# Kernel optimization log

Measured on AMD Instinct MI355X. Metric: run time of the kernel, lower is better.

The kernel has to match this reference:

```python
import jax, jax.numpy as jnp
import numpy as np

D = 1024
H = 16
HD = D // H
B = 8
S = 1024


def setup_inputs() -> dict:
    key = jax.random.key(0)
    ks = jax.random.split(key, 12)
    std = 0.02
    inp = {
        "x": jax.random.normal(ks[0], (B, S, D), jnp.float32),
        "rel_pos_enc": jax.random.normal(ks[1], (S, HD), jnp.float32) * std,
        "attention_mask": jax.random.randint(ks[2], (B, S), 0, 2, jnp.int32),
        "Wq": jax.random.normal(ks[3], (D, D), jnp.float32) * std,
        "bq": jnp.zeros((D,), jnp.float32),
        "Wk": jax.random.normal(ks[4], (D, D), jnp.float32) * std,
        "bk": jnp.zeros((D,), jnp.float32),
        "Wv": jax.random.normal(ks[5], (D, D), jnp.float32) * std,
        "bv": jnp.zeros((D,), jnp.float32),
        "Wo": jax.random.normal(ks[6], (D, D), jnp.float32) * std,
        "bo": jnp.zeros((D,), jnp.float32),
    }
    return inp


def reference(x, rel_pos_enc, attention_mask, Wq, bq, Wk, bk, Wv, bv, Wo, bo):
    b, s, d = x.shape
    scale = HD ** -0.5
    # projections + split heads -> [B, H, S, hd]
    q = (x @ Wq + bq).reshape(b, s, H, HD).transpose(0, 2, 1, 3)
    k = (x @ Wk + bk).reshape(b, s, H, HD).transpose(0, 2, 1, 3)
    v = (x @ Wv + bv).reshape(b, s, H, HD).transpose(0, 2, 1, 3)
    # content scores [B,H,S,S]
    scores = jnp.einsum("bhsd,bhtd->bhst", q, k) * scale
    # additive relative-position bias: q . rel_pos_enc[t]  -> [B,H,S,S]
    scores = scores + jnp.einsum("bhsd,td->bhst", q, rel_pos_enc)
    # key-padding mask [B,S] -> [B,1,1,S]
    scores = jnp.where(attention_mask[:, None, None, :] == 0, -jnp.inf, scores)
    attn = jax.nn.softmax(scores, axis=-1)
    ctx = jnp.einsum("bhst,bhtd->bhsd", attn, v)
    ctx = ctx.transpose(0, 2, 1, 3).reshape(b, s, d)
    return ctx @ Wo + bo
```

## Files before the change

kernel.cpp:

```cpp
#include <hip/hip_runtime.h>

#define DD 1024
#define HH 16
#define HDD 64
#define BBATCH 8
#define SS 1024
#define NROW (BBATCH*SS)
#define PSTR 72

typedef _Float16 f16x8 __attribute__((ext_vector_type(8)));
typedef _Float16 f16x4 __attribute__((ext_vector_type(4)));
typedef float    f32x4 __attribute__((ext_vector_type(4)));

__device__ __forceinline__ void async_cp16(const void* g, void* l) {
    __builtin_amdgcn_global_load_lds(
        (const __attribute__((address_space(1))) void*)g,
        (__attribute__((address_space(3))) void*)l, 16, 0, 0);
}

__global__ __launch_bounds__(256) void conv_x_kernel(
    const float* __restrict__ x, _Float16* __restrict__ xh)
{
    size_t i8 = ((size_t)blockIdx.x * 256 + threadIdx.x) * 8;
    float4 v0 = *(const float4*)&x[i8];
    float4 v1 = *(const float4*)&x[i8 + 4];
    float vf[8] = {v0.x, v0.y, v0.z, v0.w, v1.x, v1.y, v1.z, v1.w};
    f16x8 hv;
    #pragma unroll
    for (int c = 0; c < 8; c++) hv[c] = (_Float16)vf[c];
    *(f16x8*)&xh[i8] = hv;
}

__global__ __launch_bounds__(256) void conv_w_kernel(
    const float* __restrict__ Wq, const float* __restrict__ Wk,
    const float* __restrict__ Wv, const float* __restrict__ Wo,
    _Float16* __restrict__ wt, _Float16* __restrict__ wot)
{
    __shared__ float T[64][65];
    const int z = blockIdx.z;
    const float* src = (z == 0) ? Wq : (z == 1) ? Wk : (z == 2) ? Wv : Wo;
    _Float16* dh = (z < 3) ? wt + (size_t)z * 1024 * 1024 : wot;
    const int k0 = blockIdx.x * 64, n0 = blockIdx.y * 64;
    const int tid = threadIdx.x;

    #pragma unroll
    for (int rep = 0; rep < 4; rep++) {
        int e = rep * 256 + tid;
        int kr = e >> 4, nc = (e & 15) * 4;
        *(float4*)&T[kr][nc] = *(const float4*)&src[(size_t)(k0 + kr) * 1024 + n0 + nc];
    }
    __syncthreads();
    #pragma unroll
    for (int rep = 0; rep < 4; rep++) {
        int e = rep * 256 + tid;
        int nr = e >> 4, kc = (e & 15) * 4;
        f16x4 hv;
        #pragma unroll
        for (int c = 0; c < 4; c++) hv[c] = (_Float16)T[kc + c][nr];
        *(f16x4*)&dh[(size_t)(n0 + nr) * 1024 + k0 + kc] = hv;
    }
}

__global__ __launch_bounds__(256) void gemm_f16(
    const _Float16* __restrict__ Ag, const _Float16* __restrict__ Bg,
    const float* __restrict__ b0, const float* __restrict__ b1,
    const float* __restrict__ b2, const float* __restrict__ rel,
    _Float16* __restrict__ oq, _Float16* __restrict__ okh,
    _Float16* __restrict__ ovt, float* __restrict__ dOut, int mode)
{
    __shared__ _Float16 smem[8192];
    _Float16* Ah = smem;
    _Float16* Bh = smem + 4096;

    const int tid = threadIdx.x;
    const int w = tid >> 6, l = tid & 63;
    const int lane15 = l & 15, quad = l >> 4;
    const int rm = (w >> 1) * 64, cn = (w & 1) * 64;
    const size_t r0 = (size_t)blockIdx.y * 128;
    const size_t n0 = (size_t)blockIdx.x * 128;

    const int lrow = l >> 2;
    const int lko  = (l & 3) * 8;
    const int ch0 = 2 * w, ch1 = 2 * w + 1;

    f32x4 acc[4][4] = {};

    for (int ks = 0; ks < 32; ks++) {
        const size_t kofs = (size_t)ks * 32 + lko;
        __syncthreads();
        {
            const size_t ga0 = (r0 + ch0 * 16 + lrow) * 1024 + kofs;
            const size_t ga1 = (r0 + ch1 * 16 + lrow) * 1024 + kofs;
            const size_t gb0 = (n0 + ch0 * 16 + lrow) * 1024 + kofs;
            const size_t gb1 = (n0 + ch1 * 16 + lrow) * 1024 + kofs;
            async_cp16(&Ag[ga0], &Ah[ch0 * 512]);
            async_cp16(&Ag[ga1], &Ah[ch1 * 512]);
            async_cp16(&Bg[gb0], &Bh[ch0 * 512]);
            async_cp16(&Bg[gb1], &Bh[ch1 * 512]);
        }
        __syncthreads();

        f16x8 ah[4], bh4[4];
        #pragma unroll
        for (int ii = 0; ii < 4; ii++)
            ah[ii] = *(const f16x8*)&Ah[(rm + ii * 16 + lane15) * 32 + quad * 8];
        #pragma unroll
        for (int jj = 0; jj < 4; jj++)
            bh4[jj] = *(const f16x8*)&Bh[(cn + jj * 16 + lane15) * 32 + quad * 8];
        #pragma unroll
        for (int ii = 0; ii < 4; ii++)
            #pragma unroll
            for (int jj = 0; jj < 4; jj++)
                acc[ii][jj] = __builtin_amdgcn_mfma_f32_16x16x32_f16(
                    ah[ii], bh4[jj], acc[ii][jj], 0, 0, 0);
    }

    if (mode == 0) {
        const int z = blockIdx.x >> 3;
        const float* bias = (z == 0) ? b0 : (z == 1) ? b1 : b2;
        const int nbase = (blockIdx.x & 7) * 128 + cn;
        #pragma unroll
        for (int ii = 0; ii < 4; ii++)
            #pragma unroll
            for (int jj = 0; jj < 4; jj++) {
                int nc = nbase + jj * 16 + lane15;
                int hh = nc >> 6, hd = nc & 63;
                float bsv = bias[nc];
                #pragma unroll
                for (int r = 0; r < 4; r++) {
                    int gr = (int)r0 + rm + ii * 16 + quad * 4 + r;
                    int bb = gr >> 10, s = gr & 1023;
                    float val = acc[ii][jj][r] + bsv;
                    size_t hidx = (((size_t)bb * HH + hh) * SS + s) * HDD + hd;
                    if (z == 0) {
                        oq[hidx] = (_Float16)val;
                    } else if (z == 1) {
                        okh[hidx] = (_Float16)(val * 0.125f + rel[s * HDD + hd]);
                    } else {
                        ovt[(((size_t)bb * HH + hh) * HDD + hd) * SS + s] = (_Float16)val;
                    }
                }
            }
    } else {
        #pragma unroll
        for (int ii = 0; ii < 4; ii++)
            #pragma unroll
            for (int jj = 0; jj < 4; jj++) {
                int nc = (int)n0 + cn + jj * 16 + lane15;
                float bsv = b0[nc];
                #pragma unroll
                for (int r = 0; r < 4; r++) {
                    int gr = (int)r0 + rm + ii * 16 + quad * 4 + r;
                    dOut[(size_t)gr * DD + nc] = acc[ii][jj][r] + bsv;
                }
            }
    }
}

__global__ __launch_bounds__(512, 4) void attn_mfma(
    const _Float16* __restrict__ qh, const _Float16* __restrict__ kh,
    const _Float16* __restrict__ vt, const int* __restrict__ mask,
    _Float16* __restrict__ ctx)
{
    __shared__ _Float16 Kbuf[2][64 * PSTR];
    __shared__ _Float16 Vbuf[2][64 * PSTR];
    __shared__ _Float16 Ps[128 * PSTR];
    __shared__ float maddL[1024];

    const int tid = threadIdx.x;
    const int w = tid >> 6, l = tid & 63;
    const int lane15 = l & 15, quad = l >> 4;
    const int id = blockIdx.x;
    const int qt = id >> 7;
    const int bh = id & 127;
    const int b = bh >> 4, h = bh & 15;
    const size_t kbase0 = (size_t)bh * SS;
    const size_t vbase0 = (size_t)bh * HDD;
    const int qrow_blk = qt * 128 + w * 16;

    for (int i = tid; i < 1024; i += 512)
        maddL[i] = (mask[b * SS + i] == 0) ? -1e30f : 0.0f;

    f16x8 qf[2];
    #pragma unroll
    for (int ks = 0; ks < 2; ks++)
        qf[ks] = *(const f16x8*)&qh[(kbase0 + qrow_blk + lane15) * HDD + ks * 32 + quad * 8];

    f16x8 vone;
    #pragma unroll
    for (int j = 0; j < 8; j++) vone[j] = (lane15 == 0) ? (_Float16)1.0f : (_Float16)0.0f;

    f32x4 O[5] = {};

    const int grow = tid >> 3;
    const int gcc  = (tid & 7) * 8;
    const _Float16* kp = &kh[(kbase0 + grow) * HDD + gcc];
    const _Float16* vp = &vt[(vbase0 + grow) * SS + gcc];
    f16x8 kreg = *(const f16x8*)kp;
    f16x8 vreg = *(const f16x8*)vp;

    int p = 0;
    for (int kt = 0; kt < 16; kt++) {
        *(f16x8*)&Kbuf[p][grow * PSTR + gcc] = kreg;
        *(f16x8*)&Vbuf[p][grow * PSTR + gcc] = vreg;
        __syncthreads();

        const int nkt = (kt + 1) & 15;
        kreg = *(const f16x8*)(kp + (size_t)nkt * 64 * HDD);
        vreg = *(const f16x8*)(vp + (size_t)nkt * 64);

        const int t0 = kt * 64;

        f32x4 S[4];
        #pragma unroll
        for (int nt = 0; nt < 4; nt++) {
            f16x8 kf0 = *(const f16x8*)&Kbuf[p][(nt * 16 + lane15) * PSTR + quad * 8];
            f16x8 kf1 = *(const f16x8*)&Kbuf[p][(nt * 16 + lane15) * PSTR + 32 + quad * 8];
            f32x4 c = {};
            c = __builtin_amdgcn_mfma_f32_16x16x32_f16(qf[0], kf0, c, 0, 0, 0);
            c = __builtin_amdgcn_mfma_f32_16x16x32_f16(qf[1], kf1, c, 0, 0, 0);
            S[nt] = c;
        }

        const int rowb = w * 16 + quad * 4;
        #pragma unroll
        for (int nt = 0; nt < 4; nt++) {
            float madd = maddL[t0 + nt * 16 + lane15] - 3.0f;
            int colp = (nt * 16 + lane15 + 16 * quad) & 63;
            #pragma unroll
            for (int r = 0; r < 4; r++)
                Ps[(rowb + r) * PSTR + colp] = (_Float16)__expf(S[nt][r] + madd);
        }

        const int swz = 16 * (lane15 >> 2);
        #pragma unroll
        for (int ks2 = 0; ks2 < 2; ks2++) {
            int colp = (ks2 * 32 + quad * 8 + swz) & 63;
            f16x8 pf = *(const f16x8*)&Ps[(w * 16 + lane15) * PSTR + colp];
            #pragma unroll
            for (int nd = 0; nd < 4; nd++) {
                f16x8 vf = *(const f16x8*)&Vbuf[p][(nd * 16 + lane15) * PSTR + ks2 * 32 + quad * 8];
                O[nd] = __builtin_amdgcn_mfma_f32_16x16x32_f16(pf, vf, O[nd], 0, 0, 0);
            }
            O[4] = __builtin_amdgcn_mfma_f32_16x16x32_f16(pf, vone, O[4], 0, 0, 0);
        }
        p ^= 1;
    }

    float linv[4];
    #pragma unroll
    for (int r = 0; r < 4; r++) {
        float lsum = __shfl(O[4][r], l & 48, 64);
        linv[r] = 1.0f / lsum;
    }
    #pragma unroll
    for (int nd = 0; nd < 4; nd++) {
        int d = nd * 16 + lane15;
        #pragma unroll
        for (int r = 0; r < 4; r++) {
            int qrow = qt * 128 + w * 16 + quad * 4 + r;
            ctx[((size_t)b * SS + qrow) * DD + h * HDD + d] =
                (_Float16)(O[nd][r] * linv[r]);
        }
    }
}

extern "C" void kernel_launch(void* const* d_in, const int* in_sizes, int n_in,
                              void* d_out, int out_size, void* d_ws, size_t ws_size,
                              hipStream_t stream) {
    const float* x    = (const float*)d_in[0];
    const float* rel  = (const float*)d_in[1];
    const int*   mask = (const int*)d_in[2];
    const float* Wq = (const float*)d_in[3];  const float* bq = (const float*)d_in[4];
    const float* Wk = (const float*)d_in[5];  const float* bk = (const float*)d_in[6];
    const float* Wv = (const float*)d_in[7];  const float* bv = (const float*)d_in[8];
    const float* Wo = (const float*)d_in[9];  const float* bo = (const float*)d_in[10];
    float* out = (float*)d_out;

    const size_t XN = (size_t)NROW * DD;
    char* p = (char*)d_ws;
    _Float16* xh  = (_Float16*)p; p += XN * 2;
    _Float16* wt  = (_Float16*)p; p += (size_t)3072 * 1024 * 2;
    _Float16* wot = (_Float16*)p; p += (size_t)1024 * 1024 * 2;
    _Float16* qhp = (_Float16*)p; p += XN * 2;
    _Float16* khp = (_Float16*)p; p += XN * 2;
    _Float16* vtp = (_Float16*)p; p += XN * 2;
    _Float16* ctx = xh;

    conv_x_kernel<<<dim3((unsigned)(XN / 2048)), 256, 0, stream>>>(x, xh);
    conv_w_kernel<<<dim3(16, 16, 4), 256, 0, stream>>>(Wq, Wk, Wv, Wo, wt, wot);
    gemm_f16<<<dim3(24, 64), 256, 0, stream>>>(
        xh, wt, bq, bk, bv, rel, qhp, khp, vtp, nullptr, 0);
    attn_mfma<<<dim3(1024), 512, 0, stream>>>(
        qhp, khp, vtp, mask, ctx);
    gemm_f16<<<dim3(8, 64), 256, 0, stream>>>(
        ctx, wot, bo, nullptr, nullptr, nullptr,
        nullptr, nullptr, nullptr, out, 1);
}
```

Measured before the change: 316.2 us.

## Double GEMM K-tile to 64 and XOR-swizzle LDS layout

The f16 GEMM now loads a 128x64 K-slice of A and B per iteration instead of 128x32. This halves the number of barrier pairs and loop iterations. The LDS layout stores each 16-byte chunk at a position XORed with the row index, so the fragment reads for MFMA avoid bank conflicts. LDS use doubles to 32 KB per block, which may reduce occupancy.

Result: faster. 306.3 us (-3.1%).

```diff
diff --git a/kernel.cpp b/kernel.cpp
--- a/kernel.cpp
+++ b/kernel.cpp
@@ -68,9 +68,9 @@
     _Float16* __restrict__ oq, _Float16* __restrict__ okh,
     _Float16* __restrict__ ovt, float* __restrict__ dOut, int mode)
 {
-    __shared__ _Float16 smem[8192];
+    __shared__ _Float16 smem[16384];
     _Float16* Ah = smem;
-    _Float16* Bh = smem + 4096;
+    _Float16* Bh = smem + 8192;
 
     const int tid = threadIdx.x;
     const int w = tid >> 6, l = tid & 63;
@@ -79,40 +79,48 @@
     const size_t r0 = (size_t)blockIdx.y * 128;
     const size_t n0 = (size_t)blockIdx.x * 128;
 
-    const int lrow = l >> 2;
-    const int lko  = (l & 3) * 8;
-    const int ch0 = 2 * w, ch1 = 2 * w + 1;
+    const int srow = tid >> 3;
+    const int schp = tid & 7;
+    const int sch  = schp ^ (srow & 7);
 
     f32x4 acc[4][4] = {};
 
-    for (int ks = 0; ks < 32; ks++) {
-        const size_t kofs = (size_t)ks * 32 + lko;
+    for (int ks = 0; ks < 16; ks++) {
+        const int kbase = ks * 64;
         __syncthreads();
-        {
-            const size_t ga0 = (r0 + ch0 * 16 + lrow) * 1024 + kofs;
-            const size_t ga1 = (r0 + ch1 * 16 + lrow) * 1024 + kofs;
-            const size_t gb0 = (n0 + ch0 * 16 + lrow) * 1024 + kofs;
-            const size_t gb1 = (n0 + ch1 * 16 + lrow) * 1024 + kofs;
-            async_cp16(&Ag[ga0], &Ah[ch0 * 512]);
-            async_cp16(&Ag[ga1], &Ah[ch1 * 512]);
-            async_cp16(&Bg[gb0], &Bh[ch0 * 512]);
-            async_cp16(&Bg[gb1], &Bh[ch1 * 512]);
+        #pragma unroll
+        for (int i = 0; i < 4; i++) {
+            int row = i * 32 + srow;
+            int s = row * 8 + schp;
+            const size_t ga = (r0 + row) * 1024 + kbase + sch * 8;
+            const size_t gb = (n0 + row) * 1024 + kbase + sch * 8;
+            async_cp16(&Ag[ga], &Ah[s * 8]);
+            async_cp16(&Bg[gb], &Bh[s * 8]);
         }
         __syncthreads();
 
-        f16x8 ah[4], bh4[4];
-        #pragma unroll
-        for (int ii = 0; ii < 4; ii++)
-            ah[ii] = *(const f16x8*)&Ah[(rm + ii * 16 + lane15) * 32 + quad * 8];
-        #pragma unroll
-        for (int jj = 0; jj < 4; jj++)
-            bh4[jj] = *(const f16x8*)&Bh[(cn + jj * 16 + lane15) * 32 + quad * 8];
-        #pragma unroll
-        for (int ii = 0; ii < 4; ii++)
-            #pragma unroll
-            for (int jj = 0; jj < 4; jj++)
-                acc[ii][jj] = __builtin_amdgcn_mfma_f32_16x16x32_f16(
-                    ah[ii], bh4[jj], acc[ii][jj], 0, 0, 0);
+        #pragma unroll
+        for (int ksub = 0; ksub < 2; ksub++) {
+            f16x8 ah[4], bh4[4];
+            #pragma unroll
+            for (int ii = 0; ii < 4; ii++) {
+                int row = rm + ii * 16 + lane15;
+                int chp = (ksub * 4 + quad) ^ (row & 7);
+                ah[ii] = *(const f16x8*)&Ah[row * 64 + chp * 8];
+            }
+            #pragma unroll
+            for (int jj = 0; jj < 4; jj++) {
+                int col = cn + jj * 16 + lane15;
+                int chp = (ksub * 4 + quad) ^ (col & 7);
+                bh4[jj] = *(const f16x8*)&Bh[col * 64 + chp * 8];
+            }
+            #pragma unroll
+            for (int ii = 0; ii < 4; ii++)
+                #pragma unroll
+                for (int jj = 0; jj < 4; jj++)
+                    acc[ii][jj] = __builtin_amdgcn_mfma_f32_16x16x32_f16(
+                        ah[ii], bh4[jj], acc[ii][jj], 0, 0, 0);
+        }
     }
 
     if (mode == 0) {
```
